# Performance work log

Measured on AMD Instinct MI355X. Metric: run time of the kernel, lower is better.

Reference implementation:

```python
import jax, jax.numpy as jnp
import numpy as np
from jax import lax

ALPHA = 4.0  # spikingjelly default Sigmoid surrogate alpha
EPS = 1e-5

@jax.custom_vjp
def spike_fn(u):
    return (u >= 0.0).astype(u.dtype)

def _spike_fwd(u):
    return spike_fn(u), u

def _spike_bwd(u, g):
    sg = jax.nn.sigmoid(ALPHA * u)
    return (g * ALPHA * sg * (1.0 - sg),)

spike_fn.defvjp(_spike_fwd, _spike_bwd)

def if_node(x):
    """Multi-step IF neuron (v_threshold=1, hard reset to 0) over leading T dim."""
    def step(v, xt):
        v = v + xt
        s = spike_fn(v - 1.0)
        v = v * (1.0 - s)
        return v, s
    _, spikes = lax.scan(step, jnp.zeros_like(x[0]), x)
    return spikes

def layer_norm(x, g, b):
    m = jnp.mean(x, axis=-1, keepdims=True)
    var = jnp.mean((x - m) ** 2, axis=-1, keepdims=True)
    return (x - m) * lax.rsqrt(var + EPS) * g + b

def setup_inputs() -> dict:
    key = jax.random.key(0)
    T, B, S, D = 4, 8, 1024, 768
    ks = jax.random.split(key, 5)
    scale = 1.0 / np.sqrt(D)
    inp = {
        "x": jax.random.normal(ks[0], (T, B, S, D), jnp.float32),
        "wq": jax.random.normal(ks[1], (D, D), jnp.float32) * scale,
        "wk": jax.random.normal(ks[2], (D, D), jnp.float32) * scale,
        "wv": jax.random.normal(ks[3], (D, D), jnp.float32) * scale,
        "wo": jax.random.normal(ks[4], (D, D), jnp.float32) * scale,
        "gq": jnp.ones((D,), jnp.float32), "bq": jnp.zeros((D,), jnp.float32),
        "gk": jnp.ones((D,), jnp.float32), "bk": jnp.zeros((D,), jnp.float32),
        "gv": jnp.ones((D,), jnp.float32), "bv": jnp.zeros((D,), jnp.float32),
        "go": jnp.ones((D,), jnp.float32), "bo": jnp.zeros((D,), jnp.float32),
    }
    return inp

def reference(x, wq, wk, wv, wo, gq, bq, gk, bk, gv, bv, go, bo):
    T, B, S, D = x.shape
    H, HD = 12, 64
    tmp = if_node(x)                                   # [T,B,S,D] spikes
    Q = if_node(layer_norm(tmp @ wq, gq, bq))
    K = if_node(layer_norm(tmp @ wk, gk, bk))
    V = if_node(layer_norm(tmp @ wv, gv, bv))
    # [T,B,S,H,HD] -> [T,B,H,S,HD]
    Q = Q.reshape(T, B, S, H, HD).transpose(0, 1, 3, 2, 4)
    K = K.reshape(T, B, S, H, HD).transpose(0, 1, 3, 2, 4)
    V = V.reshape(T, B, S, H, HD).transpose(0, 1, 3, 2, 4)
    QK = jnp.sum(Q * K, axis=-2, keepdims=True)        # [T,B,H,1,HD]
    QK = if_node(QK)                                   # talking_heads IF spikes
    QKV = V * QK                                       # broadcast over S
    QKV = QKV.transpose(0, 1, 3, 2, 4).reshape(T, B, S, D)
    return layer_norm(QKV @ wo, go, bo)
```

## Files before the change

### kernel.cpp

```cpp
#include <hip/hip_runtime.h>
#include <hip/hip_bf16.h>

#define T_ 4
#define B_ 8
#define S_ 1024
#define D_ 768
#define BS_ (B_*S_)
#define M_ (T_*B_*S_)
#define BSD_ (B_*S_*D_)
#define LN_EPS 1e-5f
#define TAU 4e-5f
#define TAU2 2e-6f
#define ECAP (1 << 20)

typedef unsigned short u16;
typedef unsigned char u8;
typedef unsigned int u32;
typedef unsigned long long u64;
typedef __bf16 bf16x8 __attribute__((ext_vector_type(8)));
typedef float f32x4 __attribute__((ext_vector_type(4)));

__global__ __launch_bounds__(768)
void k_if_mask(const float* __restrict__ x, u64* __restrict__ Am, u16* __restrict__ Ab) {
    int bs = blockIdx.x;
    int d = threadIdx.x;
    int wv = d >> 6, lane = d & 63;
    float v = 0.f;
    for (int t = 0; t < T_; ++t) {
        v += x[(size_t)t * BSD_ + (size_t)bs * D_ + d];
        bool s = (v >= 1.0f);
        u64 m = __ballot(s);
        if (lane == 0) Am[((size_t)t * 12 + wv) * BS_ + bs] = m;
        Ab[(size_t)t * BSD_ + (size_t)bs * D_ + d] = s ? 0x3F80 : 0;
        if (s) v = 0.f;
    }
}

__global__ void k_wconv(const float* __restrict__ wq, const float* __restrict__ wk,
                        const float* __restrict__ wv, const float* __restrict__ wo,
                        u16* __restrict__ Whi, u16* __restrict__ Wlo, u16* __restrict__ Wo) {
    int idx = blockIdx.x * 256 + threadIdx.x;
    int mat = idx / (D_ * D_);
    int r = idx % (D_ * D_);
    int n = r / D_;
    int k = r % D_;
    const float* src = (mat == 0) ? wq : (mat == 1) ? wk : (mat == 2) ? wv : wo;
    float w = src[k * D_ + n];
    __bf16 hi = (__bf16)w;
    u16 uhi = __builtin_bit_cast(u16, hi);
    if (mat == 3) { Wo[r] = uhi; return; }
    float lo = w - (float)hi;
    u16 ulo = __builtin_bit_cast(u16, (__bf16)lo);
    Whi[(size_t)mat * D_ * D_ + r] = uhi;
    Wlo[(size_t)mat * D_ * D_ + r] = ulo;
}

__device__ __forceinline__ void gload16(const void* g, void* l) {
    __builtin_amdgcn_global_load_lds(
        (const __attribute__((address_space(1))) unsigned int*)g,
        (__attribute__((address_space(3))) unsigned int*)l, 16, 0, 0);
}

template<int NMATS>
__global__ __launch_bounds__(256)
void k_gemm(const u16* __restrict__ A,
            const u16* __restrict__ Bh0, const u16* __restrict__ Bl0, float* __restrict__ C0,
            const u16* __restrict__ Bh1, const u16* __restrict__ Bl1, float* __restrict__ C1,
            const u16* __restrict__ Bh2, const u16* __restrict__ Bl2, float* __restrict__ C2,
            int ntn, int N) {
    __shared__ __align__(16) u16 As[128 * 64];
    __shared__ __align__(16) u16 Bh[128 * 64];
    __shared__ __align__(16) u16 Bl[NMATS == 2 ? 128 * 64 : 8];
    int my = blockIdx.y;
    const u16* Bhi = (my == 0) ? Bh0 : (my == 1) ? Bh1 : Bh2;
    const u16* Blo = (my == 0) ? Bl0 : (my == 1) ? Bl1 : Bl2;
    float* C = (my == 0) ? C0 : (my == 1) ? C1 : C2;
    int bid = blockIdx.x;
    bid = (bid & 7) * (gridDim.x >> 3) + (bid >> 3);
    int bn = bid % ntn, bm = bid / ntn;
    int tid = threadIdx.x;
    int l = tid & 63, w = tid >> 6;
    int wr = w >> 1, wc = w & 1;
    int lan16 = l & 15, kh = l >> 4;

    f32x4 acc[4][4];
    #pragma unroll
    for (int m = 0; m < 4; ++m)
        #pragma unroll
        for (int n = 0; n < 4; ++n)
            #pragma unroll
            for (int r = 0; r < 4; ++r) acc[m][n][r] = 0.f;

    int srow[4], scol[4];
    #pragma unroll
    for (int j = 0; j < 4; ++j) {
        int li = j * 256 + tid;
        srow[j] = li >> 3;
        scol[j] = ((li & 7) ^ ((li >> 3) & 7)) * 8;
    }
    int wbase = (tid >> 6) << 10;

    int aoff[4][2], boff[4][2];
    #pragma unroll
    for (int m = 0; m < 4; ++m)
        #pragma unroll
        for (int s = 0; s < 2; ++s) {
            int Ra = wr * 64 + m * 16 + lan16;
            aoff[m][s] = Ra * 128 + (((s * 4 + kh) ^ (Ra & 7)) << 4);
            int Rb = wc * 64 + m * 16 + lan16;
            boff[m][s] = Rb * 128 + (((s * 4 + kh) ^ (Rb & 7)) << 4);
        }

    for (int kk = 0; kk < 768; kk += 64) {
        #pragma unroll
        for (int j = 0; j < 4; ++j) {
            gload16(A   + (size_t)(bm * 128 + srow[j]) * 768 + kk + scol[j],
                    (char*)As + j * 4096 + wbase);
            gload16(Bhi + (size_t)(bn * 128 + srow[j]) * 768 + kk + scol[j],
                    (char*)Bh + j * 4096 + wbase);
            if (NMATS == 2)
                gload16(Blo + (size_t)(bn * 128 + srow[j]) * 768 + kk + scol[j],
                        (char*)Bl + j * 4096 + wbase);
        }
        __syncthreads();
        #pragma unroll
        for (int s = 0; s < 2; ++s) {
            bf16x8 af[4], bh[4], bl[4];
            #pragma unroll
            for (int m = 0; m < 4; ++m)
                af[m] = *(const bf16x8*)((const char*)As + aoff[m][s]);
            #pragma unroll
            for (int n = 0; n < 4; ++n) {
                bh[n] = *(const bf16x8*)((const char*)Bh + boff[n][s]);
                if (NMATS == 2) bl[n] = *(const bf16x8*)((const char*)Bl + boff[n][s]);
            }
            #pragma unroll
            for (int m = 0; m < 4; ++m)
                #pragma unroll
                for (int n = 0; n < 4; ++n) {
                    acc[m][n] = __builtin_amdgcn_mfma_f32_16x16x32_bf16(af[m], bh[n], acc[m][n], 0, 0, 0);
                    if (NMATS == 2)
                        acc[m][n] = __builtin_amdgcn_mfma_f32_16x16x32_bf16(af[m], bl[n], acc[m][n], 0, 0, 0);
                }
        }
        __syncthreads();
    }
    #pragma unroll
    for (int m = 0; m < 4; ++m)
        #pragma unroll
        for (int n = 0; n < 4; ++n)
            #pragma unroll
            for (int r = 0; r < 4; ++r) {
                int crow = bm * 128 + wr * 64 + m * 16 + kh * 4 + r;
                int ccol = bn * 128 + wc * 64 + n * 16 + lan16;
                C[(size_t)crow * N + ccol] = acc[m][n][r];
            }
}

__global__ __launch_bounds__(256)
void k_lnif(const float* __restrict__ Y0, const float* __restrict__ Y1,
            const float* __restrict__ Y2,
            const float* __restrict__ gq, const float* __restrict__ bq,
            const float* __restrict__ gk, const float* __restrict__ bk,
            const float* __restrict__ gv, const float* __restrict__ bv,
            u8* __restrict__ Qs, u8* __restrict__ Ks, u8* __restrict__ Vs,
            float2* __restrict__ MI, u32* __restrict__ elist, int* __restrict__ ecnt,
            int mat0) {
    #pragma clang fp contract(off)
    int mat = mat0 + blockIdx.y;
    const float* Y = (mat == 0) ? Y0 : (mat == 1) ? Y1 : Y2;
    const float* g = (mat == 0) ? gq : (mat == 1) ? gk : gv;
    const float* bt = (mat == 0) ? bq : (mat == 1) ? bk : bv;
    u8* Sp = (mat == 0) ? Qs : (mat == 1) ? Ks : Vs;
    int row = blockIdx.x * 4 + (threadIdx.x >> 6);
    int lane = threadIdx.x & 63;
    float v[12];
    bool fl[12];
    #pragma unroll
    for (int i = 0; i < 12; ++i) { v[i] = 0.f; fl[i] = false; }
    float gv_[12], bv_[12];
    #pragma unroll
    for (int i = 0; i < 12; ++i) { gv_[i] = g[lane + 64*i]; bv_[i] = bt[lane + 64*i]; }
    for (int t = 0; t < T_; ++t) {
        size_t base = ((size_t)t * BS_ + row) * D_;
        float xv[12];
        double s = 0.0;
        #pragma unroll
        for (int i = 0; i < 12; ++i) { xv[i] = Y[base + lane + 64*i]; s += (double)xv[i]; }
        #pragma unroll
        for (int o = 1; o < 64; o <<= 1) s += __shfl_xor(s, o, 64);
        s = __shfl(s, 0, 64);
        float m = (float)(s / 768.0);
        float d[12];
        double q = 0.0;
        #pragma unroll
        for (int i = 0; i < 12; ++i) { d[i] = xv[i] - m; float sq = d[i]*d[i]; q += (double)sq; }
        #pragma unroll
        for (int o = 1; o < 64; o <<= 1) q += __shfl_xor(q, o, 64);
        q = __shfl(q, 0, 64);
        float var = (float)(q / 768.0);
        float inv = 1.0f / __fsqrt_rn(var + LN_EPS);
        if (lane == 0) MI[((size_t)mat * 4 + t) * BS_ + row] = make_float2(m, inv);
        #pragma unroll
        for (int i = 0; i < 12; ++i) {
            float yn = ((d[i] * inv) * gv_[i]) + bv_[i];
            v[i] += yn;
            fl[i] = fl[i] || (fabsf(v[i] - 1.0f) < TAU);
            bool sp = (v[i] >= 1.0f);
            Sp[base + lane + 64*i] = sp ? (u8)1 : (u8)0;
            if (sp) v[i] = 0.f;
        }
    }
    #pragma unroll
    for (int i = 0; i < 12; ++i) {
        if (fl[i]) {
            int slot = atomicAdd(ecnt, 1);
            if (slot < ECAP)
                elist[slot] = ((u32)mat << 23) | ((u32)row << 10) | (u32)(lane + 64*i);
        }
    }
}

__global__ __launch_bounds__(256)
void k_repair2(const u64* __restrict__ Am,
               const float* __restrict__ wq, const float* __restrict__ wk,
               const float* __restrict__ wv, const float2* __restrict__ MI,
               const float* __restrict__ gq, const float* __restrict__ bq,
               const float* __restrict__ gk, const float* __restrict__ bk,
               const float* __restrict__ gv, const float* __restrict__ bv,
               u8* __restrict__ Qs, u8* __restrict__ Ks, u8* __restrict__ Vs,
               const u32* __restrict__ elist, const int* __restrict__ ecnt,
               int* __restrict__ rowlist2, int* __restrict__ cnt2) {
    #pragma clang fp contract(off)
    int nf = *ecnt;
    if (nf > ECAP) nf = ECAP;
    int t = threadIdx.x & 3;
    int gid = (blockIdx.x * 256 + threadIdx.x) >> 2;
    int ngroups = (gridDim.x * 256) >> 2;
    int lane = threadIdx.x & 63;
    int gbase = lane & ~3;
    for (int e = gid; e < nf; e += ngroups) {
        u32 p = elist[e];
        int mat = p >> 23;
        int row = (p >> 10) & 0x1FFF;
        int col = p & 0x3FF;
        const float* W = (mat == 0) ? wq : (mat == 1) ? wk : wv;
        const float* g = (mat == 0) ? gq : (mat == 1) ? gk : gv;
        const float* bb = (mat == 0) ? bq : (mat == 1) ? bk : bv;
        u8* Sp = (mat == 0) ? Qs : (mat == 1) ? Ks : Vs;
        float y = 0.f;
        for (int kw = 0; kw < 12; ++kw) {
            u64 m = Am[((size_t)t * 12 + kw) * BS_ + row];
            const float* wp = W + (size_t)(kw * 64) * D_ + col;
            #pragma unroll 16
            for (int kb = 0; kb < 64; ++kb) {
                float w = wp[(size_t)kb * D_];
                y += ((m >> kb) & 1ull) ? w : 0.0f;
            }
        }
        float y0 = __shfl(y, gbase + 0, 64);
        float y1 = __shfl(y, gbase + 1, 64);
        float y2 = __shfl(y, gbase + 2, 64);
        float y3 = __shfl(y, gbase + 3, 64);
        float yt[4] = {y0, y1, y2, y3};
        float gc = g[col], bc = bb[col];
        float v = 0.f;
        bool efl = false;
        #pragma unroll
        for (int tt = 0; tt < 4; ++tt) {
            float2 mi = MI[((size_t)mat * 4 + tt) * BS_ + row];
            float yn = (((yt[tt] - mi.x) * mi.y) * gc) + bc;
            v += yn;
            efl = efl || (fabsf(v - 1.0f) < TAU2);
            bool sp = (v >= 1.0f);
            if (tt == t)
                Sp[((size_t)tt * BS_ + row) * D_ + col] = sp ? (u8)1 : (u8)0;
            if (sp) v = 0.f;
        }
        if (efl && t == 0) {
            int slot = atomicAdd(cnt2 + mat, 1);
            rowlist2[mat * BS_ + slot] = row;
        }
    }
}

__global__ __launch_bounds__(768)
void k_repairT(const u64* __restrict__ Am,
               const float* __restrict__ wq, const float* __restrict__ wk,
               const float* __restrict__ wv,
               const float* __restrict__ gq, const float* __restrict__ bq,
               const float* __restrict__ gk, const float* __restrict__ bk,
               const float* __restrict__ gv, const float* __restrict__ bv,
               u8* __restrict__ Qs, u8* __restrict__ Ks, u8* __restrict__ Vs,
               const int* __restrict__ rowlist, const int* __restrict__ cnt) {
    #pragma clang fp contract(off)
    int mat = blockIdx.y;
    int nf = cnt[mat];
    const float* W = (mat == 0) ? wq : (mat == 1) ? wk : wv;
    const float* g = (mat == 0) ? gq : (mat == 1) ? gk : gv;
    const float* bb = (mat == 0) ? bq : (mat == 1) ? bk : bv;
    u8* Sp = (mat == 0) ? Qs : (mat == 1) ? Ks : Vs;
    const float4* Wv4 = (const float4*)W;

    __shared__ u64 mks[4][12];
    __shared__ int pops[4][12];
    __shared__ int cnt4[4];
    __shared__ u16 idxs[4][768];
    __shared__ float4 ys[4][192];
    __shared__ float2 mi_sh[4];
    __shared__ double redd[12];

    int tid = threadIdx.x;
    int t = tid / 192;
    int tg = tid % 192;

    for (int e = blockIdx.x; e < nf; e += gridDim.x) {
        int row = rowlist[mat * BS_ + e];

        if (tid < 48) {
            int tt = tid / 12, kw = tid % 12;
            u64 m = Am[((size_t)tt * 12 + kw) * BS_ + row];
            mks[tt][kw] = m;
            pops[tt][kw] = __popcll(m);
        }
        __syncthreads();
        if (tid < 48) {
            int tt = tid / 12, kw = tid % 12;
            int off = 0;
            for (int j = 0; j < kw; ++j) off += pops[tt][j];
            u64 m = mks[tt][kw];
            int kb0 = kw * 64;
            while (m) {
                int kb = __builtin_ctzll(m);
                m &= m - 1;
                idxs[tt][off++] = (u16)(kb0 + kb);
            }
            if (kw == 11) cnt4[tt] = off;
        }
        __syncthreads();

        int cn = cnt4[t];
        float y0 = 0.f, y1 = 0.f, y2 = 0.f, y3 = 0.f;
        const u16* il = idxs[t];
        #pragma unroll 8
        for (int i = 0; i < cn; ++i) {
            float4 w = Wv4[(size_t)il[i] * 192 + tg];
            y0 += w.x; y1 += w.y; y2 += w.z; y3 += w.w;
        }

        int lane = tid & 63;
        int wv_t = tg >> 6;
        double s = (double)y0 + (double)y1 + (double)y2 + (double)y3;
        #pragma unroll
        for (int o = 1; o < 64; o <<= 1) s += __shfl_xor(s, o, 64);
        if (lane == 0) redd[t * 3 + wv_t] = s;
        __syncthreads();
        double stot = redd[t * 3] + redd[t * 3 + 1] + redd[t * 3 + 2];
        float mean = (float)(stot / 768.0);
        float d0 = y0 - mean, d1 = y1 - mean, d2 = y2 - mean, d3 = y3 - mean;
        double q = (double)(d0*d0) + (double)(d1*d1) + (double)(d2*d2) + (double)(d3*d3);
        #pragma unroll
        for (int o = 1; o < 64; o <<= 1) q += __shfl_xor(q, o, 64);
        __syncthreads();
        if (lane == 0) redd[t * 3 + wv_t] = q;
        __syncthreads();
        double qtot = redd[t * 3] + redd[t * 3 + 1] + redd[t * 3 + 2];
        float var = (float)(qtot / 768.0);
        float inv = 1.0f / __fsqrt_rn(var + LN_EPS);

        ys[t][tg] = make_float4(y0, y1, y2, y3);
        if (tg == 0) mi_sh[t] = make_float2(mean, inv);
        __syncthreads();

        if (tid < 192) {
            float4 gd = ((const float4*)g)[tg];
            float4 bd = ((const float4*)bb)[tg];
            float4 yt[4];
            float2 mi[4];
            #pragma unroll
            for (int tt = 0; tt < 4; ++tt) { yt[tt] = ys[tt][tg]; mi[tt] = mi_sh[tt]; }
            uchar4 o4[4];
            #pragma unroll
            for (int j = 0; j < 4; ++j) {
                float gj = (j == 0) ? gd.x : (j == 1) ? gd.y : (j == 2) ? gd.z : gd.w;
                float bj = (j == 0) ? bd.x : (j == 1) ? bd.y : (j == 2) ? bd.z : bd.w;
                float v = 0.f;
                #pragma unroll
                for (int tt = 0; tt < 4; ++tt) {
                    float yj = (j == 0) ? yt[tt].x : (j == 1) ? yt[tt].y : (j == 2) ? yt[tt].z : yt[tt].w;
                    float d = yj - mi[tt].x;
                    float yn = ((d * mi[tt].y) * gj) + bj;
                    v += yn;
                    bool sp = (v >= 1.0f);
                    u8 sb = sp ? (u8)1 : (u8)0;
                    if (j == 0) o4[tt].x = sb;
                    if (j == 1) o4[tt].y = sb;
                    if (j == 2) o4[tt].z = sb;
                    if (j == 3) o4[tt].w = sb;
                    if (sp) v = 0.f;
                }
            }
            #pragma unroll
            for (int tt = 0; tt < 4; ++tt)
                *(uchar4*)(Sp + ((size_t)tt * BS_ + row) * D_ + tg * 4) = o4[tt];
        }
        __syncthreads();
    }
}

__global__ void k_qkred(const u8* __restrict__ Q, const u8* __restrict__ K,
                        float* __restrict__ QK) {
    int bid = blockIdx.x;
    int sg = bid & 31, tb = bid >> 5;
    int tid = threadIdx.x;
    int c4 = tid * 4;
    size_t base = (size_t)tb * S_ * D_ + (size_t)sg * 32 * D_;
    int acc[4] = {0, 0, 0, 0};
    for (int s = 0; s < 32; ++s) {
        uchar4 q = *(const uchar4*)(Q + base + (size_t)s * D_ + c4);
        uchar4 k = *(const uchar4*)(K + base + (size_t)s * D_ + c4);
        acc[0] += q.x & k.x; acc[1] += q.y & k.y; acc[2] += q.z & k.z; acc[3] += q.w & k.w;
    }
    float* dst = QK + (size_t)tb * D_ + c4;
    #pragma unroll
    for (int j = 0; j < 4; ++j) atomicAdd(dst + j, (float)acc[j]);
}

__global__ void k_qkif(const float* __restrict__ QK, u8* __restrict__ QKs) {
    int i = blockIdx.x * 256 + threadIdx.x;
    float v = 0.f;
    for (int t = 0; t < T_; ++t) {
        v += QK[t * (B_ * D_) + i];
        bool s = (v >= 1.0f);
        QKs[t * (B_ * D_) + i] = s ? 1 : 0;
        if (s) v = 0.f;
    }
}

__global__ void k_qkv(const u8* __restrict__ V, const u8* __restrict__ QKs,
                      u16* __restrict__ O) {
    size_t e = ((size_t)blockIdx.x * 256 + threadIdx.x) * 4;
    uchar4 v = *(const uchar4*)(V + e);
    size_t d = e % D_;
    size_t b = (e / ((size_t)S_ * D_)) % B_;
    size_t t = e / BSD_;
    uchar4 qk = *(const uchar4*)(QKs + t * (B_ * D_) + b * D_ + d);
    ushort4 o;
    o.x = (v.x & qk.x) ? 0x3F80 : 0;
    o.y = (v.y & qk.y) ? 0x3F80 : 0;
    o.z = (v.z & qk.z) ? 0x3F80 : 0;
    o.w = (v.w & qk.w) ? 0x3F80 : 0;
    *(ushort4*)(O + e) = o;
}

__device__ __forceinline__ float block_sum(float v, float* red) {
    #pragma unroll
    for (int o = 32; o > 0; o >>= 1) v += __shfl_down(v, o, 64);
    int lane = threadIdx.x & 63, w = threadIdx.x >> 6;
    __syncthreads();
    if (lane == 0) red[w] = v;
    __syncthreads();
    return (red[0] + red[1]) + (red[2] + red[3]);
}

__global__ __launch_bounds__(256)
void k_lnfinal(const float* __restrict__ Y, const float* __restrict__ g,
               const float* __restrict__ bt, float* __restrict__ out) {
    #pragma clang fp contract(off)
    __shared__ float red[4];
    size_t row = (size_t)blockIdx.x * D_;
    int tid = threadIdx.x;
    float y[3];
    float s = 0.f;
    #pragma unroll
    for (int j = 0; j < 3; ++j) { y[j] = Y[row + tid + j * 256]; s += y[j]; }
    float mean = block_sum(s, red) / 768.0f;
    float q = 0.f;
    #pragma unroll
    for (int j = 0; j < 3; ++j) { float d = y[j] - mean; q += d * d; }
    float var = block_sum(q, red) / 768.0f;
    float inv = 1.0f / __fsqrt_rn(var + LN_EPS);
    #pragma unroll
    for (int j = 0; j < 3; ++j) {
        int c = tid + j * 256;
        out[row + c] = (y[j] - mean) * inv * g[c] + bt[c];
    }
}

extern "C" void kernel_launch(void* const* d_in, const int* in_sizes, int n_in,
                              void* d_out, int out_size, void* d_ws, size_t ws_size,
                              hipStream_t stream) {
    const float* x  = (const float*)d_in[0];
    const float* wq = (const float*)d_in[1];
    const float* wk = (const float*)d_in[2];
    const float* wv = (const float*)d_in[3];
    const float* wo = (const float*)d_in[4];
    const float* gq = (const float*)d_in[5];
    const float* bq = (const float*)d_in[6];
    const float* gk = (const float*)d_in[7];
    const float* bk = (const float*)d_in[8];
    const float* gv = (const float*)d_in[9];
    const float* bv = (const float*)d_in[10];
    const float* go = (const float*)d_in[11];
    const float* bo = (const float*)d_in[12];
    float* out = (float*)d_out;

    char* ws = (char*)d_ws;
    size_t off = 0;
    auto alloc = [&](size_t bytes) -> void* {
        void* p = ws + off;
        off += (bytes + 255) & ~(size_t)255;
        return p;
    };
    u64* Am    = (u64*)alloc((size_t)T_ * 12 * BS_ * 8);
    u16* Ab    = (u16*)alloc((size_t)M_ * D_ * 2);
    float* Y0  = (float*)alloc((size_t)M_ * D_ * 4);
    u8* Qs     = (u8*)alloc((size_t)M_ * D_);
    u8* Ks     = (u8*)alloc((size_t)M_ * D_);
    u8* Vs     = (u8*)alloc((size_t)M_ * D_);
    u16* Whi   = (u16*)alloc((size_t)3 * D_ * D_ * 2);
    u16* Wlo   = (u16*)alloc((size_t)3 * D_ * D_ * 2);
    u16* Wo    = (u16*)alloc((size_t)D_ * D_ * 2);
    float* QK  = (float*)alloc((size_t)T_ * B_ * D_ * 4);
    u8* QKs    = (u8*)alloc((size_t)T_ * B_ * D_);
    float2* MI = (float2*)alloc((size_t)3 * 4 * BS_ * 8);
    u32* elist = (u32*)alloc((size_t)ECAP * 4);
    int* rowlist2 = (int*)alloc((size_t)3 * BS_ * 4);
    int* cnt   = (int*)alloc(256);
    float* Y1  = (float*)alloc((size_t)M_ * D_ * 4);
    float* Y2  = (float*)alloc((size_t)M_ * D_ * 4);
    bool fused = (off <= ws_size);
    if (!fused) { Y1 = Y0; Y2 = Y0; }
    int* cnt2 = cnt;
    int* ecnt = cnt + 3;

    hipMemsetAsync(QK, 0, (size_t)T_ * B_ * D_ * 4, stream);
    hipMemsetAsync(cnt, 0, 256, stream);

    k_if_mask<<<BS_, 768, 0, stream>>>(x, Am, Ab);
    k_wconv<<<(4 * D_ * D_) / 256, 256, 0, stream>>>(wq, wk, wv, wo, Whi, Wlo, Wo);
    const int ntn = D_ / 128;
    const int gemm_grid = (M_ / 128) * ntn;
    const u16* WhiQ = Whi + 0 * D_ * D_; const u16* WloQ = Wlo + 0 * D_ * D_;
    const u16* WhiK = Whi + 1 * D_ * D_; const u16* WloK = Wlo + 1 * D_ * D_;
    const u16* WhiV = Whi + 2 * D_ * D_; const u16* WloV = Wlo + 2 * D_ * D_;
    if (fused) {
        k_gemm<2><<<dim3(gemm_grid, 3), 256, 0, stream>>>(Ab,
            WhiQ, WloQ, Y0, WhiK, WloK, Y1, WhiV, WloV, Y2, ntn, D_);
        k_lnif<<<dim3(BS_ / 4, 3), 256, 0, stream>>>(Y0, Y1, Y2,
            gq, bq, gk, bk, gv, bv, Qs, Ks, Vs, MI, elist, ecnt, 0);
    } else {
        k_gemm<2><<<dim3(gemm_grid, 1), 256, 0, stream>>>(Ab,
            WhiQ, WloQ, Y0, WhiQ, WloQ, Y0, WhiQ, WloQ, Y0, ntn, D_);
        k_lnif<<<dim3(BS_ / 4, 1), 256, 0, stream>>>(Y0, Y0, Y0,
            gq, bq, gk, bk, gv, bv, Qs, Ks, Vs, MI, elist, ecnt, 0);
        k_gemm<2><<<dim3(gemm_grid, 1), 256, 0, stream>>>(Ab,
            WhiK, WloK, Y0, WhiK, WloK, Y0, WhiK, WloK, Y0, ntn, D_);
        k_lnif<<<dim3(BS_ / 4, 1), 256, 0, stream>>>(Y0, Y0, Y0,
            gq, bq, gk, bk, gv, bv, Qs, Ks, Vs, MI, elist, ecnt, 1);
        k_gemm<2><<<dim3(gemm_grid, 1), 256, 0, stream>>>(Ab,
            WhiV, WloV, Y0, WhiV, WloV, Y0, WhiV, WloV, Y0, ntn, D_);
        k_lnif<<<dim3(BS_ / 4, 1), 256, 0, stream>>>(Y0, Y0, Y0,
            gq, bq, gk, bk, gv, bv, Qs, Ks, Vs, MI, elist, ecnt, 2);
    }
    k_repair2<<<512, 256, 0, stream>>>(Am, wq, wk, wv, MI, gq, bq, gk, bk, gv, bv,
                                       Qs, Ks, Vs, elist, ecnt, rowlist2, cnt2);
    k_repairT<<<dim3(256, 3), 768, 0, stream>>>(Am, wq, wk, wv, gq, bq, gk, bk, gv, bv,
                                                Qs, Ks, Vs, rowlist2, cnt2);
    k_qkred<<<T_ * B_ * 32, 192, 0, stream>>>(Qs, Ks, QK);
    k_qkif<<<(B_ * D_) / 256, 256, 0, stream>>>(QK, QKs);
    k_qkv<<<(M_ * D_) / 4 / 256, 256, 0, stream>>>(Vs, QKs, Ab);
    k_gemm<1><<<dim3(gemm_grid, 1), 256, 0, stream>>>(Ab,
        Wo, Wo, Y0, Wo, Wo, Y0, Wo, Wo, Y0, ntn, D_);
    k_lnfinal<<<M_, 256, 0, stream>>>(Y0, go, bo, out);
}
```

Measured before the change: 558.9 us.

## Feed GEMM A-operand from packed spike bitmasks via LDS lookup table

Binary spike activations are no longer materialised as a dense bf16 matrix. Each GEMM block loads the per-row 64-bit spike masks into LDS and expands them on the fly into bf16x8 fragments through a 256-entry LUT. The mask layout becomes row-major across k-words, and the QKV product now emits masks instead of bf16. This removes large A-operand global writes and reads, in exchange for extra LDS lookups with possible bank conflicts and a little more ALU work in the GEMM inner loop.

```diff
diff --git a/kernel.cpp b/kernel.cpp
--- a/kernel.cpp
+++ b/kernel.cpp
@@ -21,7 +21,7 @@
 typedef float f32x4 __attribute__((ext_vector_type(4)));
 
 __global__ __launch_bounds__(768)
-void k_if_mask(const float* __restrict__ x, u64* __restrict__ Am, u16* __restrict__ Ab) {
+void k_if_mask(const float* __restrict__ x, u64* __restrict__ Am2) {
     int bs = blockIdx.x;
     int d = threadIdx.x;
     int wv = d >> 6, lane = d & 63;
@@ -30,8 +30,7 @@
         v += x[(size_t)t * BSD_ + (size_t)bs * D_ + d];
         bool s = (v >= 1.0f);
         u64 m = __ballot(s);
-        if (lane == 0) Am[((size_t)t * 12 + wv) * BS_ + bs] = m;
-        Ab[(size_t)t * BSD_ + (size_t)bs * D_ + d] = s ? 0x3F80 : 0;
+        if (lane == 0) Am2[((size_t)t * BS_ + bs) * 12 + wv] = m;
         if (s) v = 0.f;
     }
 }
@@ -63,14 +62,15 @@
 
 template<int NMATS>
 __global__ __launch_bounds__(256)
-void k_gemm(const u16* __restrict__ A,
+void k_gemm(const u64* __restrict__ Amask_g,
             const u16* __restrict__ Bh0, const u16* __restrict__ Bl0, float* __restrict__ C0,
             const u16* __restrict__ Bh1, const u16* __restrict__ Bl1, float* __restrict__ C1,
             const u16* __restrict__ Bh2, const u16* __restrict__ Bl2, float* __restrict__ C2,
             int ntn, int N) {
-    __shared__ __align__(16) u16 As[128 * 64];
     __shared__ __align__(16) u16 Bh[128 * 64];
     __shared__ __align__(16) u16 Bl[NMATS == 2 ? 128 * 64 : 8];
+    __shared__ __align__(16) u64 Amsk[128 * 13];
+    __shared__ __align__(16) u32 LUT[256 * 4];
     int my = blockIdx.y;
     const u16* Bhi = (my == 0) ? Bh0 : (my == 1) ? Bh1 : Bh2;
     const u16* Blo = (my == 0) ? Bl0 : (my == 1) ? Bl1 : Bl2;
@@ -83,6 +83,22 @@
     int wr = w >> 1, wc = w & 1;
     int lan16 = l & 15, kh = l >> 4;
 
+    {
+        int e = tid;
+        u32 w0 = (((e >> 0) & 1) ? 0x3F80u : 0u) | (((e >> 1) & 1) ? 0x3F800000u : 0u);
+        u32 w1 = (((e >> 2) & 1) ? 0x3F80u : 0u) | (((e >> 3) & 1) ? 0x3F800000u : 0u);
+        u32 w2 = (((e >> 4) & 1) ? 0x3F80u : 0u) | (((e >> 5) & 1) ? 0x3F800000u : 0u);
+        u32 w3 = (((e >> 6) & 1) ? 0x3F80u : 0u) | (((e >> 7) & 1) ? 0x3F800000u : 0u);
+        LUT[e * 4 + 0] = w0; LUT[e * 4 + 1] = w1;
+        LUT[e * 4 + 2] = w2; LUT[e * 4 + 3] = w3;
+    }
+    #pragma unroll
+    for (int j = 0; j < 6; ++j) {
+        int idx = tid + j * 256;
+        int r = idx / 12, kw = idx % 12;
+        Amsk[r * 13 + kw] = Amask_g[(size_t)(bm * 128 + r) * 12 + kw];
+    }
+
     f32x4 acc[4][4];
     #pragma unroll
     for (int m = 0; m < 4; ++m)
@@ -100,22 +116,22 @@
     }
     int wbase = (tid >> 6) << 10;
 
-    int aoff[4][2], boff[4][2];
-    #pragma unroll
-    for (int m = 0; m < 4; ++m)
+    int arow[4], boff[4][2];
+    #pragma unroll
+    for (int m = 0; m < 4; ++m) arow[m] = (wr * 64 + m * 16 + lan16) * 13;
+    #pragma unroll
+    for (int n = 0; n < 4; ++n)
         #pragma unroll
         for (int s = 0; s < 2; ++s) {
-            int Ra = wr * 64 + m * 16 + lan16;
-            aoff[m][s] = Ra * 128 + (((s * 4 + kh) ^ (Ra & 7)) << 4);
-            int Rb = wc * 64 + m * 16 + lan16;
-            boff[m][s] = Rb * 128 + (((s * 4 + kh) ^ (Rb & 7)) << 4);
-        }
-
-    for (int kk = 0; kk < 768; kk += 64) {
+            int Rb = wc * 64 + n * 16 + lan16;
+            boff[n][s] = Rb * 128 + (((s * 4 + kh) ^ (Rb & 7)) << 4);
+        }
+    const char* LUTb = (const char*)LUT;
+
+    for (int kw = 0; kw < 12; ++kw) {
+        int kk = kw * 64;
         #pragma unroll
         for (int j = 0; j < 4; ++j) {
-            gload16(A   + (size_t)(bm * 128 + srow[j]) * 768 + kk + scol[j],
-                    (char*)As + j * 4096 + wbase);
             gload16(Bhi + (size_t)(bn * 128 + srow[j]) * 768 + kk + scol[j],
                     (char*)Bh + j * 4096 + wbase);
             if (NMATS == 2)
@@ -123,12 +139,17 @@
                         (char*)Bl + j * 4096 + wbase);
         }
         __syncthreads();
+        u64 mA[4];
+        #pragma unroll
+        for (int m = 0; m < 4; ++m) mA[m] = Amsk[arow[m] + kw];
         #pragma unroll
         for (int s = 0; s < 2; ++s) {
             bf16x8 af[4], bh[4], bl[4];
             #pragma unroll
-            for (int m = 0; m < 4; ++m)
-                af[m] = *(const bf16x8*)((const char*)As + aoff[m][s]);
+            for (int m = 0; m < 4; ++m) {
+                u32 byt = (u32)(mA[m] >> (s * 32 + kh * 8)) & 0xFFu;
+                af[m] = *(const bf16x8*)(LUTb + byt * 16);
+            }
             #pragma unroll
             for (int n = 0; n < 4; ++n) {
                 bh[n] = *(const bf16x8*)((const char*)Bh + boff[n][s]);
@@ -222,7 +243,7 @@
 }
 
 __global__ __launch_bounds__(256)
-void k_repair2(const u64* __restrict__ Am,
+void k_repair2(const u64* __restrict__ Am2,
                const float* __restrict__ wq, const float* __restrict__ wk,
                const float* __restrict__ wv, const float2* __restrict__ MI,
                const float* __restrict__ gq, const float* __restrict__ bq,
@@ -250,7 +271,7 @@
         u8* Sp = (mat == 0) ? Qs : (mat == 1) ? Ks : Vs;
         float y = 0.f;
         for (int kw = 0; kw < 12; ++kw) {
-            u64 m = Am[((size_t)t * 12 + kw) * BS_ + row];
+            u64 m = Am2[((size_t)t * BS_ + row) * 12 + kw];
             const float* wp = W + (size_t)(kw * 64) * D_ + col;
             #pragma unroll 16
             for (int kb = 0; kb < 64; ++kb) {
@@ -285,7 +306,7 @@
 }
 
 __global__ __launch_bounds__(768)
-void k_repairT(const u64* __restrict__ Am,
+void k_repairT(const u64* __restrict__ Am2,
                const float* __restrict__ wq, const float* __restrict__ wk,
                const float* __restrict__ wv,
                const float* __restrict__ gq, const float* __restrict__ bq,
@@ -319,7 +340,7 @@
 
         if (tid < 48) {
             int tt = tid / 12, kw = tid % 12;
-            u64 m = Am[((size_t)tt * 12 + kw) * BS_ + row];
+            u64 m = Am2[((size_t)tt * BS_ + row) * 12 + kw];
             mks[tt][kw] = m;
             pops[tt][kw] = __popcll(m);
         }
@@ -437,20 +458,17 @@
     }
 }
 
-__global__ void k_qkv(const u8* __restrict__ V, const u8* __restrict__ QKs,
-                      u16* __restrict__ O) {
-    size_t e = ((size_t)blockIdx.x * 256 + threadIdx.x) * 4;
-    uchar4 v = *(const uchar4*)(V + e);
-    size_t d = e % D_;
-    size_t b = (e / ((size_t)S_ * D_)) % B_;
-    size_t t = e / BSD_;
-    uchar4 qk = *(const uchar4*)(QKs + t * (B_ * D_) + b * D_ + d);
-    ushort4 o;
-    o.x = (v.x & qk.x) ? 0x3F80 : 0;
-    o.y = (v.y & qk.y) ? 0x3F80 : 0;
-    o.z = (v.z & qk.z) ? 0x3F80 : 0;
-    o.w = (v.w & qk.w) ? 0x3F80 : 0;
-    *(ushort4*)(O + e) = o;
+__global__ __launch_bounds__(768)
+void k_qkvmask(const u8* __restrict__ Vs, const u8* __restrict__ QKs,
+               u64* __restrict__ Am3) {
+    int row = blockIdx.x;
+    int d = threadIdx.x;
+    int wv = d >> 6, lane = d & 63;
+    int t = row >> 13;
+    int b = (row & (BS_ - 1)) >> 10;
+    u8 v = Vs[(size_t)row * D_ + d] & QKs[t * (B_ * D_) + b * D_ + d];
+    u64 m = __ballot(v != 0);
+    if (lane == 0) Am3[(size_t)row * 12 + wv] = m;
 }
 
 __device__ __forceinline__ float block_sum(float v, float* red) {
@@ -512,8 +530,8 @@
         off += (bytes + 255) & ~(size_t)255;
         return p;
     };
-    u64* Am    = (u64*)alloc((size_t)T_ * 12 * BS_ * 8);
-    u16* Ab    = (u16*)alloc((size_t)M_ * D_ * 2);
+    u64* Am2   = (u64*)alloc((size_t)M_ * 12 * 8);
+    u64* Am3   = (u64*)alloc((size_t)M_ * 12 * 8);
     float* Y0  = (float*)alloc((size_t)M_ * D_ * 4);
     u8* Qs     = (u8*)alloc((size_t)M_ * D_);
     u8* Ks     = (u8*)alloc((size_t)M_ * D_);
@@ -537,7 +555,7 @@
     hipMemsetAsync(QK, 0, (size_t)T_ * B_ * D_ * 4, stream);
     hipMemsetAsync(cnt, 0, 256, stream);
 
-    k_if_mask<<<BS_, 768, 0, stream>>>(x, Am, Ab);
+    k_if_mask<<<BS_, 768, 0, stream>>>(x, Am2);
     k_wconv<<<(4 * D_ * D_) / 256, 256, 0, stream>>>(wq, wk, wv, wo, Whi, Wlo, Wo);
     const int ntn = D_ / 128;
     const int gemm_grid = (M_ / 128) * ntn;
@@ -545,32 +563,32 @@
     const u16* WhiK = Whi + 1 * D_ * D_; const u16* WloK = Wlo + 1 * D_ * D_;
     const u16* WhiV = Whi + 2 * D_ * D_; const u16* WloV = Wlo + 2 * D_ * D_;
     if (fused) {
-        k_gemm<2><<<dim3(gemm_grid, 3), 256, 0, stream>>>(Ab,
+        k_gemm<2><<<dim3(gemm_grid, 3), 256, 0, stream>>>(Am2,
             WhiQ, WloQ, Y0, WhiK, WloK, Y1, WhiV, WloV, Y2, ntn, D_);
         k_lnif<<<dim3(BS_ / 4, 3), 256, 0, stream>>>(Y0, Y1, Y2,
             gq, bq, gk, bk, gv, bv, Qs, Ks, Vs, MI, elist, ecnt, 0);
     } else {
-        k_gemm<2><<<dim3(gemm_grid, 1), 256, 0, stream>>>(Ab,
+        k_gemm<2><<<dim3(gemm_grid, 1), 256, 0, stream>>>(Am2,
             WhiQ, WloQ, Y0, WhiQ, WloQ, Y0, WhiQ, WloQ, Y0, ntn, D_);
         k_lnif<<<dim3(BS_ / 4, 1), 256, 0, stream>>>(Y0, Y0, Y0,
             gq, bq, gk, bk, gv, bv, Qs, Ks, Vs, MI, elist, ecnt, 0);
-        k_gemm<2><<<dim3(gemm_grid, 1), 256, 0, stream>>>(Ab,
+        k_gemm<2><<<dim3(gemm_grid, 1), 256, 0, stream>>>(Am2,
             WhiK, WloK, Y0, WhiK, WloK, Y0, WhiK, WloK, Y0, ntn, D_);
         k_lnif<<<dim3(BS_ / 4, 1), 256, 0, stream>>>(Y0, Y0, Y0,
             gq, bq, gk, bk, gv, bv, Qs, Ks, Vs, MI, elist, ecnt, 1);
-        k_gemm<2><<<dim3(gemm_grid, 1), 256, 0, stream>>>(Ab,
+        k_gemm<2><<<dim3(gemm_grid, 1), 256, 0, stream>>>(Am2,
             WhiV, WloV, Y0, WhiV, WloV, Y0, WhiV, WloV, Y0, ntn, D_);
         k_lnif<<<dim3(BS_ / 4, 1), 256, 0, stream>>>(Y0, Y0, Y0,
             gq, bq, gk, bk, gv, bv, Qs, Ks, Vs, MI, elist, ecnt, 2);
     }
-    k_repair2<<<512, 256, 0, stream>>>(Am, wq, wk, wv, MI, gq, bq, gk, bk, gv, bv,
+    k_repair2<<<512, 256, 0, stream>>>(Am2, wq, wk, wv, MI, gq, bq, gk, bk, gv, bv,
                                        Qs, Ks, Vs, elist, ecnt, rowlist2, cnt2);
-    k_repairT<<<dim3(256, 3), 768, 0, stream>>>(Am, wq, wk, wv, gq, bq, gk, bk, gv, bv,
+    k_repairT<<<dim3(256, 3), 768, 0, stream>>>(Am2, wq, wk, wv, gq, bq, gk, bk, gv, bv,
                                                 Qs, Ks, Vs, rowlist2, cnt2);
     k_qkred<<<T_ * B_ * 32, 192, 0, stream>>>(Qs, Ks, QK);
     k_qkif<<<(B_ * D_) / 256, 256, 0, stream>>>(QK, QKs);
-    k_qkv<<<(M_ * D_) / 4 / 256, 256, 0, stream>>>(Vs, QKs, Ab);
-    k_gemm<1><<<dim3(gemm_grid, 1), 256, 0, stream>>>(Ab,
+    k_qkvmask<<<M_, 768, 0, stream>>>(Vs, QKs, Am3);
+    k_gemm<1><<<dim3(gemm_grid, 1), 256, 0, stream>>>(Am3,
         Wo, Wo, Y0, Wo, Wo, Y0, Wo, Wo, Y0, ntn, D_);
     k_lnfinal<<<M_, 256, 0, stream>>>(Y0, go, bo, out);
 }
```

Result: slower. 576.2 us (+3.1%).
